# Kernel tuning notes

Measured on AMD Instinct MI355X. Metric: run time of the kernel, lower is better.

The kernel has to match this reference:

```python
import jax, jax.numpy as jnp
import numpy as np

B, T, C, H = 512, 512, 64, 128  # batch, timesteps, n_channel, n_hidden


def setup_inputs() -> dict:
    key = jax.random.key(0)
    k_x, k_wa, k_wi, k_we = jax.random.split(key, 4)
    x = jax.random.normal(k_x, (B, T, C), dtype=jnp.float32)
    # keras 'uniform' initializer: U(-0.05, 0.05)
    weight_att = jax.random.uniform(k_wa, (H, C, C), jnp.float32, -0.05, 0.05)
    weight_input = jax.random.uniform(k_wi, (H, C, C), jnp.float32, -0.05, 0.05)
    weight_e = jax.random.uniform(k_we, (H, C, C), jnp.float32, -0.05, 0.05)
    return {"x": x, "weight_att": weight_att, "weight_input": weight_input,
            "weight_e": weight_e}


def reference(x, weight_att, weight_input, weight_e):
    b, t, c = x.shape
    h = weight_input.shape[0]
    # initial attention state: ones / n_channel  -> [B, H, C]
    att0 = jnp.full((b, h, c), 1.0 / c, dtype=x.dtype)

    def step(att, x_t):
        # batch_mult(weight_input, x_t): out[b,h,c] = sum_k x_t[b,k] * W[h,c,k]
        a = jnp.einsum('bk,hck->bhc', x_t, weight_input)
        # batch_att_mult(weight_att, att): out[b,h,c] = sum_k att[b,h,k] * W[h,c,k]
        a = a + jnp.einsum('bhk,hck->bhc', att, weight_att)
        a = jnp.tanh(a)
        a = jnp.einsum('bhk,hck->bhc', a, weight_e)
        a = jax.nn.softmax(a, axis=-1)
        # reduce_sum(matmul(att [B,H,C], x [B,C,1]), -1) -> [B,H]
        out_t = jnp.einsum('bhc,bc->bh', a, x_t)
        return a, out_t

    xs = jnp.swapaxes(x, 0, 1)  # [T, B, C] for scan over time
    _, outs = jax.lax.scan(step, att0, xs)  # outs: [T, B, H]
    return jnp.swapaxes(outs, 0, 1)  # [B, T, H]
```

## Files before the change

kernel.cpp:

```cpp
#include <hip/hip_runtime.h>


constexpr int Bsz = 512, Tsz = 512, Csz = 64, Hsz = 128;

typedef __attribute__((ext_vector_type(8))) short short8;
typedef __attribute__((may_alias)) short8 short8m;
typedef __attribute__((ext_vector_type(4))) float f32x4;
typedef __attribute__((ext_vector_type(2))) unsigned int u32x2;
typedef __attribute__((may_alias)) u32x2 u32x2m;

#define LOG2E     1.44269504088896f
#define SCALE_CAT 2.88539008177793f

#define XT 0
#define AT 2304
#define YT 4608
#define OBF 6912
#define ROWB 144
#define OPITCH 20

__device__ __forceinline__ unsigned short f2bf_rn(float f) {
    return (unsigned short)((__float_as_uint(f) + 0x8000u) >> 16);
}
__device__ __forceinline__ unsigned int pkbf(float lo, float hi) {
    unsigned int r;
    asm("v_cvt_pk_bf16_f32 %0, %1, %2" : "=v"(r) : "v"(lo), "v"(hi));
    return r;
}
template<int CTRL>
__device__ __forceinline__ float dpp_add(float v) {
    int t = __builtin_amdgcn_update_dpp(0, __float_as_int(v), CTRL, 0xF, 0xF, true);
    return v + __int_as_float(t);
}
__device__ __forceinline__ float row_sum16(float v) {
    v = dpp_add<0x128>(v);
    v = dpp_add<0x124>(v);
    v = dpp_add<0x4E>(v);
    v = dpp_add<0xB1>(v);
    return v;
}

__global__ __launch_bounds__(256, 4)
void x_to_bf16_perm(const float* __restrict__ x, unsigned short* __restrict__ xb) {
    int g = blockIdx.x * 256 + threadIdx.x;
    int row = g >> 3, k = g & 7;
    int b = row >> 9, t = row & 511;
    const float* src = x + (size_t)row * 64;
    short8 f;
#pragma unroll
    for (int a = 0; a < 4; ++a) {
        float2 w = *(const float2*)(src + a * 16 + 2 * k);
        f[a]     = (short)f2bf_rn(w.x);
        f[4 + a] = (short)f2bf_rn(w.y);
    }
    size_t ob = ((size_t)((b >> 4) * Tsz + t) * 16 + (b & 15)) * 64 + k * 8;
    *(short8m*)(xb + ob) = f;
}

template<bool XPRE, bool OUTWS>
__global__ __launch_bounds__(256, 4)
void attn_scan(const float* __restrict__ xg,
               const unsigned short* __restrict__ xbg,
               const float* __restrict__ w_att,
               const float* __restrict__ w_in,
               const float* __restrict__ w_e,
               float* __restrict__ outg,
               float* __restrict__ outws)
{
    __shared__ __align__(16) unsigned short wefs[4096];
    __shared__ __align__(16) char priv[4][8192];

    const int h     = blockIdx.x & (Hsz - 1);
    const int btg   = blockIdx.x >> 7;
    const int wave  = threadIdx.x >> 6;
    const int lane  = threadIdx.x & 63;
    const int btile = btg * 4 + wave;
    const int b0    = btile * 16;

    const int l15  = lane & 15;
    const int quad = lane >> 4;
    const int rowb = quad * 4;
    const int sr   = lane >> 2;
    const int lq   = lane & 3;

    {
        const float* weh = w_e + (size_t)h * Csz * Csz;
#pragma unroll
        for (int i = 0; i < 2; ++i) {
            int tp = threadIdx.x * 2 + i;
            int ntks = tp >> 6, q = (tp >> 4) & 3, l = tp & 15;
            int ks = ntks & 1;
            int nt = ntks >> 1;
            int m = ks * 4 + q;
            const float* srcw = weh + (nt * 16 + l) * 64;
            short8 f;
#pragma unroll
            for (int j = 0; j < 8; ++j) {
                int kk = ((j & 3) << 4) + 2 * m + (j >> 2);
                f[j] = (short)f2bf_rn(srcw[kk] * LOG2E);
            }
            *(short8m*)(wefs + tp * 8) = f;
        }
    }

    short8 wcat[4][4];
    {
        const float* winh = w_in  + (size_t)h * Csz * Csz;
        const float* wath = w_att + (size_t)h * Csz * Csz;
#pragma unroll
        for (int nt = 0; nt < 4; ++nt) {
            const int c = nt * 16 + l15;
#pragma unroll
            for (int ks = 0; ks < 4; ++ks) {
                const float* srcw = ((ks < 2) ? winh : wath) + c * 64;
                const int m = (ks & 1) * 4 + quad;
                short8 f;
#pragma unroll
                for (int j = 0; j < 8; ++j) {
                    int kk = ((j & 3) << 4) + 2 * m + (j >> 2);
                    f[j] = (short)f2bf_rn(srcw[kk] * SCALE_CAT);
                }
                wcat[nt][ks] = f;
            }
        }
    }

    __syncthreads();

    char* wb  = priv[wave];
    char* wbr = wb + l15 * ROWB + quad * 16;
    char* wbd = wb + quad * (4 * ROWB) + l15 * 8;
    const unsigned short* wfp = wefs + quad * 128 + l15 * 8;
    float* ob = (float*)(wb + OBF);

    {
        short8 kinit;
#pragma unroll
        for (int j = 0; j < 8; ++j) kinit[j] = (short)0x3C80;
#pragma unroll
        for (int i = 0; i < 3; ++i) {
            int idx = i * 64 + lane;
            if (idx < 144) *(short8m*)(wb + AT + idx * 16) = kinit;
        }
    }

    {
        char* st = wb + XT + sr * ROWB + lq * 32;
        if (XPRE) {
            const unsigned short* xp = xbg + ((size_t)(btile * Tsz + 0) * 16 + sr) * 64 + lq * 16;
            *(short8m*)st        = *(const short8m*)xp;
            *(short8m*)(st + 16) = *(const short8m*)(xp + 8);
        } else {
            const float* xp = xg + ((size_t)(b0 + sr) * Tsz + 0) * 64 + lq * 4;
            float4 f0 = *(const float4*)(xp);
            float4 f1 = *(const float4*)(xp + 16);
            float4 f2 = *(const float4*)(xp + 32);
            float4 f3 = *(const float4*)(xp + 48);
            short8 lo, hi;
            lo[0]=(short)f2bf_rn(f0.x); lo[1]=(short)f2bf_rn(f1.x);
            lo[2]=(short)f2bf_rn(f2.x); lo[3]=(short)f2bf_rn(f3.x);
            lo[4]=(short)f2bf_rn(f0.y); lo[5]=(short)f2bf_rn(f1.y);
            lo[6]=(short)f2bf_rn(f2.y); lo[7]=(short)f2bf_rn(f3.y);
            hi[0]=(short)f2bf_rn(f0.z); hi[1]=(short)f2bf_rn(f1.z);
            hi[2]=(short)f2bf_rn(f2.z); hi[3]=(short)f2bf_rn(f3.z);
            hi[4]=(short)f2bf_rn(f0.w); hi[5]=(short)f2bf_rn(f1.w);
            hi[6]=(short)f2bf_rn(f2.w); hi[7]=(short)f2bf_rn(f3.w);
            *(short8m*)st = lo; *(short8m*)(st + 16) = hi;
        }
    }

    float rinv[4] = {1.f, 1.f, 1.f, 1.f};

    for (int t = 0; t < Tsz; ++t) {
        const int tn = (t < Tsz - 1) ? t + 1 : t;
        short8 pxa, pxb;
        float4 pf0, pf1, pf2, pf3;
        if (XPRE) {
            const unsigned short* xp = xbg + ((size_t)(btile * Tsz + tn) * 16 + sr) * 64 + lq * 16;
            pxa = *(const short8m*)xp;
            pxb = *(const short8m*)(xp + 8);
        } else {
            const float* xp = xg + ((size_t)(b0 + sr) * Tsz + tn) * 64 + lq * 4;
            pf0 = *(const float4*)(xp);      pf1 = *(const float4*)(xp + 16);
            pf2 = *(const float4*)(xp + 32); pf3 = *(const float4*)(xp + 48);
        }

        f32x4 vacc[4];
        {
            short8 aa0 = *(const short8m*)(wbr + AT);
            short8 aa1 = *(const short8m*)(wbr + AT + 64);
            f32x4 z = {0.f, 0.f, 0.f, 0.f};
#pragma unroll
            for (int nt = 0; nt < 4; ++nt) {
                vacc[nt] = __builtin_amdgcn_mfma_f32_16x16x32_bf16(aa0, wcat[nt][2], z, 0, 0, 0);
                vacc[nt] = __builtin_amdgcn_mfma_f32_16x16x32_bf16(aa1, wcat[nt][3], vacc[nt], 0, 0, 0);
            }
            short8 ax0 = *(const short8m*)(wbr + XT);
            short8 ax1 = *(const short8m*)(wbr + XT + 64);
#pragma unroll
            for (int nt = 0; nt < 4; ++nt)
#pragma unroll
                for (int rg = 0; rg < 4; ++rg)
                    vacc[nt][rg] *= rinv[rg];
#pragma unroll
            for (int nt = 0; nt < 4; ++nt) {
                vacc[nt] = __builtin_amdgcn_mfma_f32_16x16x32_bf16(ax0, wcat[nt][0], vacc[nt], 0, 0, 0);
                vacc[nt] = __builtin_amdgcn_mfma_f32_16x16x32_bf16(ax1, wcat[nt][1], vacc[nt], 0, 0, 0);
            }
        }

#pragma unroll
        for (int rg = 0; rg < 4; ++rg) {
            float E0 = __builtin_amdgcn_exp2f(vacc[0][rg]);
            float E1 = __builtin_amdgcn_exp2f(vacc[1][rg]);
            float E2 = __builtin_amdgcn_exp2f(vacc[2][rg]);
            float E3 = __builtin_amdgcn_exp2f(vacc[3][rg]);
            float y0 = fmaf(-2.f, __builtin_amdgcn_rcpf(E0 + 1.f), 1.f);
            float y1 = fmaf(-2.f, __builtin_amdgcn_rcpf(E1 + 1.f), 1.f);
            float y2 = fmaf(-2.f, __builtin_amdgcn_rcpf(E2 + 1.f), 1.f);
            float y3 = fmaf(-2.f, __builtin_amdgcn_rcpf(E3 + 1.f), 1.f);
            u32x2 d;
            d[0] = pkbf(y0, y1);
            d[1] = pkbf(y2, y3);
            *(u32x2m*)(wbd + YT + rg * ROWB) = d;
        }

        {
            short8 y0 = *(const short8m*)(wbr + YT);
            short8 y1 = *(const short8m*)(wbr + YT + 64);
            f32x4 z = {0.f, 0.f, 0.f, 0.f};
#pragma unroll
            for (int nt = 0; nt < 4; ++nt) {
                short8 w0 = *(const short8m*)(wfp + (nt * 2) * 512);
                short8 w1 = *(const short8m*)(wfp + (nt * 2 + 1) * 512);
                vacc[nt] = __builtin_amdgcn_mfma_f32_16x16x32_bf16(y0, w0, z, 0, 0, 0);
                vacc[nt] = __builtin_amdgcn_mfma_f32_16x16x32_bf16(y1, w1, vacc[nt], 0, 0, 0);
            }
        }

        float ssum[4], dsum[4];
#pragma unroll
        for (int rg = 0; rg < 4; ++rg) {
            u32x2 xd = *(const u32x2m*)(wbd + XT + rg * ROWB);
            float xv0 = __uint_as_float(xd[0] << 16);
            float xv1 = __uint_as_float(xd[0] & 0xffff0000u);
            float xv2 = __uint_as_float(xd[1] << 16);
            float xv3 = __uint_as_float(xd[1] & 0xffff0000u);
            float p0 = __builtin_amdgcn_exp2f(vacc[0][rg]);
            float p1 = __builtin_amdgcn_exp2f(vacc[1][rg]);
            float p2 = __builtin_amdgcn_exp2f(vacc[2][rg]);
            float p3 = __builtin_amdgcn_exp2f(vacc[3][rg]);
            u32x2 d;
            d[0] = pkbf(p0, p1);
            d[1] = pkbf(p2, p3);
            *(u32x2m*)(wbd + AT + rg * ROWB) = d;
            ssum[rg] = (p0 + p1) + (p2 + p3);
            dsum[rg] = fmaf(p0, xv0, fmaf(p1, xv1, fmaf(p2, xv2, p3 * xv3)));
        }
        float oval[4];
#pragma unroll
        for (int rg = 0; rg < 4; ++rg) {
            float s = row_sum16(ssum[rg]);
            float d = row_sum16(dsum[rg]);
            rinv[rg] = __builtin_amdgcn_rcpf(s);
            oval[rg] = d * rinv[rg];
        }

        if (l15 < 4) {
            float v = oval[0];
            v = (l15 == 1) ? oval[1] : v;
            v = (l15 == 2) ? oval[2] : v;
            v = (l15 == 3) ? oval[3] : v;
            if (OUTWS) {
                ob[(rowb + l15) * OPITCH + (t & 15)] = v;
            } else {
                outg[(size_t)(b0 + rowb + l15) * (Tsz * Hsz) + (size_t)t * Hsz + h] = v;
            }
        }
        if (OUTWS && ((t & 15) == 15)) {
            float4 v = *(const float4*)&ob[sr * OPITCH + lq * 4];
            *(float4*)&outws[((size_t)h * Bsz + b0 + sr) * Tsz + (t - 15) + lq * 4] = v;
        }

        char* st = wb + XT + sr * ROWB + lq * 32;
        if (XPRE) {
            *(short8m*)st = pxa; *(short8m*)(st + 16) = pxb;
        } else {
            short8 lo, hi;
            lo[0]=(short)f2bf_rn(pf0.x); lo[1]=(short)f2bf_rn(pf1.x);
            lo[2]=(short)f2bf_rn(pf2.x); lo[3]=(short)f2bf_rn(pf3.x);
            lo[4]=(short)f2bf_rn(pf0.y); lo[5]=(short)f2bf_rn(pf1.y);
            lo[6]=(short)f2bf_rn(pf2.y); lo[7]=(short)f2bf_rn(pf3.y);
            hi[0]=(short)f2bf_rn(pf0.z); hi[1]=(short)f2bf_rn(pf1.z);
            hi[2]=(short)f2bf_rn(pf2.z); hi[3]=(short)f2bf_rn(pf3.z);
            hi[4]=(short)f2bf_rn(pf0.w); hi[5]=(short)f2bf_rn(pf1.w);
            hi[6]=(short)f2bf_rn(pf2.w); hi[7]=(short)f2bf_rn(pf3.w);
            *(short8m*)st = lo; *(short8m*)(st + 16) = hi;
        }
    }
}

__global__ __launch_bounds__(256, 4)
void out_transpose(const float* __restrict__ ws, float* __restrict__ outg) {
    __shared__ float tile[64][65];
    const int t0 = blockIdx.x * 64;
    const int h0 = blockIdx.y * 64;
    const int b  = blockIdx.z;
    const int tx = threadIdx.x & 63;
    const int wy = threadIdx.x >> 6;
#pragma unroll
    for (int i = 0; i < 16; ++i) {
        int hr = wy * 16 + i;
        tile[hr][tx] = ws[((size_t)(h0 + hr) * Bsz + b) * Tsz + t0 + tx];
    }
    __syncthreads();
#pragma unroll
    for (int i = 0; i < 16; ++i) {
        int tt = wy * 16 + i;
        outg[((size_t)b * Tsz + t0 + tt) * Hsz + h0 + tx] = tile[tx][tt];
    }
}

extern "C" void kernel_launch(void* const* d_in, const int* in_sizes, int n_in,
                              void* d_out, int out_size, void* d_ws, size_t ws_size,
                              hipStream_t stream) {
    const float* x     = (const float*)d_in[0];
    const float* w_att = (const float*)d_in[1];
    const float* w_in  = (const float*)d_in[2];
    const float* w_e   = (const float*)d_in[3];
    float* out = (float*)d_out;

    const size_t XB = (size_t)Bsz * Tsz * Csz * sizeof(unsigned short);
    const size_t OB = (size_t)Bsz * Tsz * Hsz * sizeof(float);
    unsigned short* xb  = (unsigned short*)d_ws;
    float*          ows = (float*)((char*)d_ws + XB);

    const int xblocks = Bsz * Tsz * 8 / 256;
    dim3 scan_grid(Hsz * (Bsz / 64));

    if (ws_size >= XB + OB) {
        x_to_bf16_perm<<<xblocks, 256, 0, stream>>>(x, xb);
        attn_scan<true, true><<<scan_grid, 256, 0, stream>>>(x, xb, w_att, w_in, w_e, out, ows);
        dim3 tg(Tsz / 64, Hsz / 64, Bsz);
        out_transpose<<<tg, 256, 0, stream>>>(ows, out);
    } else if (ws_size >= XB) {
        x_to_bf16_perm<<<xblocks, 256, 0, stream>>>(x, xb);
        attn_scan<true, false><<<scan_grid, 256, 0, stream>>>(x, xb, w_att, w_in, w_e, out, nullptr);
    } else {
        attn_scan<false, false><<<scan_grid, 256, 0, stream>>>(x, nullptr, w_att, w_in, w_e, out, nullptr);
    }
}
```

Before: 1.501 ms.

## Compute softmax sums and x-dot via MFMA, keep x fragments in registers

Replaces the DPP row reductions for the softmax denominator and the x-weighted sum with extra MFMA calls. These multiply the bf16 probability tile by a ones vector and by the x fragment, and only the diagonal lanes are used for the output. The x tile is now loaded straight into MFMA operand registers each step instead of being staged through LDS, which shrinks the per-wave LDS area and drops the LDS output staging buffer. Outputs are written directly per step rather than batched into float4 stores. The sums now come from bf16-rounded probabilities, and most of the dot-product MFMA output is discarded.

```diff
diff --git a/kernel.cpp b/kernel.cpp
--- a/kernel.cpp
+++ b/kernel.cpp
@@ -12,12 +12,9 @@
 #define LOG2E     1.44269504088896f
 #define SCALE_CAT 2.88539008177793f
 
-#define XT 0
-#define AT 2304
-#define YT 4608
-#define OBF 6912
+#define AT 0
+#define YT 2304
 #define ROWB 144
-#define OPITCH 20
 
 __device__ __forceinline__ unsigned short f2bf_rn(float f) {
     return (unsigned short)((__float_as_uint(f) + 0x8000u) >> 16);
@@ -26,18 +23,6 @@
     unsigned int r;
     asm("v_cvt_pk_bf16_f32 %0, %1, %2" : "=v"(r) : "v"(lo), "v"(hi));
     return r;
-}
-template<int CTRL>
-__device__ __forceinline__ float dpp_add(float v) {
-    int t = __builtin_amdgcn_update_dpp(0, __float_as_int(v), CTRL, 0xF, 0xF, true);
-    return v + __int_as_float(t);
-}
-__device__ __forceinline__ float row_sum16(float v) {
-    v = dpp_add<0x128>(v);
-    v = dpp_add<0x124>(v);
-    v = dpp_add<0x4E>(v);
-    v = dpp_add<0xB1>(v);
-    return v;
 }
 
 __global__ __launch_bounds__(256, 4)
@@ -55,6 +40,22 @@
     }
     size_t ob = ((size_t)((b >> 4) * Tsz + t) * 16 + (b & 15)) * 64 + k * 8;
     *(short8m*)(xb + ob) = f;
+}
+
+__device__ __forceinline__ void load_xfrag_f32(const float* src, int quad,
+                                               short8& f0, short8& f1) {
+#pragma unroll
+    for (int hh = 0; hh < 2; ++hh) {
+        short8 f;
+        const int K = hh * 8 + quad * 2;
+#pragma unroll
+        for (int m = 0; m < 4; ++m) {
+            float2 w = *(const float2*)(src + K + 16 * m);
+            f[m]     = (short)f2bf_rn(w.x);
+            f[m + 4] = (short)f2bf_rn(w.y);
+        }
+        if (hh == 0) f0 = f; else f1 = f;
+    }
 }
 
 template<bool XPRE, bool OUTWS>
@@ -68,7 +69,7 @@
                float* __restrict__ outws)
 {
     __shared__ __align__(16) unsigned short wefs[4096];
-    __shared__ __align__(16) char priv[4][8192];
+    __shared__ __align__(16) char priv[4][4608];
 
     const int h     = blockIdx.x & (Hsz - 1);
     const int btg   = blockIdx.x >> 7;
@@ -80,8 +81,6 @@
     const int l15  = lane & 15;
     const int quad = lane >> 4;
     const int rowb = quad * 4;
-    const int sr   = lane >> 2;
-    const int lq   = lane & 3;
 
     {
         const float* weh = w_e + (size_t)h * Csz * Csz;
@@ -131,7 +130,10 @@
     char* wbr = wb + l15 * ROWB + quad * 16;
     char* wbd = wb + quad * (4 * ROWB) + l15 * 8;
     const unsigned short* wfp = wefs + quad * 128 + l15 * 8;
-    float* ob = (float*)(wb + OBF);
+
+    short8 ones8;
+#pragma unroll
+    for (int j = 0; j < 8; ++j) ones8[j] = (short)0x3F80;
 
     {
         short8 kinit;
@@ -144,45 +146,35 @@
         }
     }
 
-    {
-        char* st = wb + XT + sr * ROWB + lq * 32;
-        if (XPRE) {
-            const unsigned short* xp = xbg + ((size_t)(btile * Tsz + 0) * 16 + sr) * 64 + lq * 16;
-            *(short8m*)st        = *(const short8m*)xp;
-            *(short8m*)(st + 16) = *(const short8m*)(xp + 8);
-        } else {
-            const float* xp = xg + ((size_t)(b0 + sr) * Tsz + 0) * 64 + lq * 4;
-            float4 f0 = *(const float4*)(xp);
-            float4 f1 = *(const float4*)(xp + 16);
-            float4 f2 = *(const float4*)(xp + 32);
-            float4 f3 = *(const float4*)(xp + 48);
-            short8 lo, hi;
-            lo[0]=(short)f2bf_rn(f0.x); lo[1]=(short)f2bf_rn(f1.x);
-            lo[2]=(short)f2bf_rn(f2.x); lo[3]=(short)f2bf_rn(f3.x);
-            lo[4]=(short)f2bf_rn(f0.y); lo[5]=(short)f2bf_rn(f1.y);
-            lo[6]=(short)f2bf_rn(f2.y); lo[7]=(short)f2bf_rn(f3.y);
-            hi[0]=(short)f2bf_rn(f0.z); hi[1]=(short)f2bf_rn(f1.z);
-            hi[2]=(short)f2bf_rn(f2.z); hi[3]=(short)f2bf_rn(f3.z);
-            hi[4]=(short)f2bf_rn(f0.w); hi[5]=(short)f2bf_rn(f1.w);
-            hi[6]=(short)f2bf_rn(f2.w); hi[7]=(short)f2bf_rn(f3.w);
-            *(short8m*)st = lo; *(short8m*)(st + 16) = hi;
-        }
+    const unsigned short* xfp = nullptr;
+    if (XPRE)
+        xfp = xbg + (size_t)btile * Tsz * 1024 + l15 * 64 + quad * 8;
+
+    const int  k3     = l15 & 3;
+    const int  orow   = rowb + k3;
+    const bool isdiag = ((l15 >> 2) == quad);
+    float* op;
+    if (OUTWS) op = outws + ((size_t)h * Bsz + b0 + orow) * Tsz;
+    else       op = outg + (size_t)(b0 + orow) * (Tsz * Hsz) + h;
+
+    short8 axc0, axc1;
+    if (XPRE) {
+        axc0 = *(const short8m*)(xfp);
+        axc1 = *(const short8m*)(xfp + 32);
+    } else {
+        load_xfrag_f32(xg + ((size_t)(b0 + l15) * Tsz) * 64, quad, axc0, axc1);
     }
 
     float rinv[4] = {1.f, 1.f, 1.f, 1.f};
 
     for (int t = 0; t < Tsz; ++t) {
         const int tn = (t < Tsz - 1) ? t + 1 : t;
-        short8 pxa, pxb;
-        float4 pf0, pf1, pf2, pf3;
+        short8 axn0, axn1;
         if (XPRE) {
-            const unsigned short* xp = xbg + ((size_t)(btile * Tsz + tn) * 16 + sr) * 64 + lq * 16;
-            pxa = *(const short8m*)xp;
-            pxb = *(const short8m*)(xp + 8);
+            axn0 = *(const short8m*)(xfp + (size_t)tn * 1024);
+            axn1 = *(const short8m*)(xfp + (size_t)tn * 1024 + 32);
         } else {
-            const float* xp = xg + ((size_t)(b0 + sr) * Tsz + tn) * 64 + lq * 4;
-            pf0 = *(const float4*)(xp);      pf1 = *(const float4*)(xp + 16);
-            pf2 = *(const float4*)(xp + 32); pf3 = *(const float4*)(xp + 48);
+            load_xfrag_f32(xg + ((size_t)(b0 + l15) * Tsz + tn) * 64, quad, axn0, axn1);
         }
 
         f32x4 vacc[4];
@@ -195,8 +187,6 @@
                 vacc[nt] = __builtin_amdgcn_mfma_f32_16x16x32_bf16(aa0, wcat[nt][2], z, 0, 0, 0);
                 vacc[nt] = __builtin_amdgcn_mfma_f32_16x16x32_bf16(aa1, wcat[nt][3], vacc[nt], 0, 0, 0);
             }
-            short8 ax0 = *(const short8m*)(wbr + XT);
-            short8 ax1 = *(const short8m*)(wbr + XT + 64);
 #pragma unroll
             for (int nt = 0; nt < 4; ++nt)
 #pragma unroll
@@ -204,8 +194,8 @@
                     vacc[nt][rg] *= rinv[rg];
 #pragma unroll
             for (int nt = 0; nt < 4; ++nt) {
-                vacc[nt] = __builtin_amdgcn_mfma_f32_16x16x32_bf16(ax0, wcat[nt][0], vacc[nt], 0, 0, 0);
-                vacc[nt] = __builtin_amdgcn_mfma_f32_16x16x32_bf16(ax1, wcat[nt][1], vacc[nt], 0, 0, 0);
+                vacc[nt] = __builtin_amdgcn_mfma_f32_16x16x32_bf16(axc0, wcat[nt][0], vacc[nt], 0, 0, 0);
+                vacc[nt] = __builtin_amdgcn_mfma_f32_16x16x32_bf16(axc1, wcat[nt][1], vacc[nt], 0, 0, 0);
             }
         }
 
@@ -238,14 +228,8 @@
             }
         }
 
-        float ssum[4], dsum[4];
 #pragma unroll
         for (int rg = 0; rg < 4; ++rg) {
-            u32x2 xd = *(const u32x2m*)(wbd + XT + rg * ROWB);
-            float xv0 = __uint_as_float(xd[0] << 16);
-            float xv1 = __uint_as_float(xd[0] & 0xffff0000u);
-            float xv2 = __uint_as_float(xd[1] << 16);
-            float xv3 = __uint_as_float(xd[1] & 0xffff0000u);
             float p0 = __builtin_amdgcn_exp2f(vacc[0][rg]);
             float p1 = __builtin_amdgcn_exp2f(vacc[1][rg]);
             float p2 = __builtin_amdgcn_exp2f(vacc[2][rg]);
@@ -254,49 +238,37 @@
             d[0] = pkbf(p0, p1);
             d[1] = pkbf(p2, p3);
             *(u32x2m*)(wbd + AT + rg * ROWB) = d;
-            ssum[rg] = (p0 + p1) + (p2 + p3);
-            dsum[rg] = fmaf(p0, xv0, fmaf(p1, xv1, fmaf(p2, xv2, p3 * xv3)));
-        }
-        float oval[4];
-#pragma unroll
-        for (int rg = 0; rg < 4; ++rg) {
-            float s = row_sum16(ssum[rg]);
-            float d = row_sum16(dsum[rg]);
-            rinv[rg] = __builtin_amdgcn_rcpf(s);
-            oval[rg] = d * rinv[rg];
-        }
-
-        if (l15 < 4) {
-            float v = oval[0];
-            v = (l15 == 1) ? oval[1] : v;
-            v = (l15 == 2) ? oval[2] : v;
-            v = (l15 == 3) ? oval[3] : v;
-            if (OUTWS) {
-                ob[(rowb + l15) * OPITCH + (t & 15)] = v;
-            } else {
-                outg[(size_t)(b0 + rowb + l15) * (Tsz * Hsz) + (size_t)t * Hsz + h] = v;
-            }
-        }
-        if (OUTWS && ((t & 15) == 15)) {
-            float4 v = *(const float4*)&ob[sr * OPITCH + lq * 4];
-            *(float4*)&outws[((size_t)h * Bsz + b0 + sr) * Tsz + (t - 15) + lq * 4] = v;
-        }
-
-        char* st = wb + XT + sr * ROWB + lq * 32;
-        if (XPRE) {
-            *(short8m*)st = pxa; *(short8m*)(st + 16) = pxb;
-        } else {
-            short8 lo, hi;
-            lo[0]=(short)f2bf_rn(pf0.x); lo[1]=(short)f2bf_rn(pf1.x);
-            lo[2]=(short)f2bf_rn(pf2.x); lo[3]=(short)f2bf_rn(pf3.x);
-            lo[4]=(short)f2bf_rn(pf0.y); lo[5]=(short)f2bf_rn(pf1.y);
-            lo[6]=(short)f2bf_rn(pf2.y); lo[7]=(short)f2bf_rn(pf3.y);
-            hi[0]=(short)f2bf_rn(pf0.z); hi[1]=(short)f2bf_rn(pf1.z);
-            hi[2]=(short)f2bf_rn(pf2.z); hi[3]=(short)f2bf_rn(pf3.z);
-            hi[4]=(short)f2bf_rn(pf0.w); hi[5]=(short)f2bf_rn(pf1.w);
-            hi[6]=(short)f2bf_rn(pf2.w); hi[7]=(short)f2bf_rn(pf3.w);
-            *(short8m*)st = lo; *(short8m*)(st + 16) = hi;
-        }
+        }
+
+        {
+            short8 pa0 = *(const short8m*)(wbr + AT);
+            short8 pa1 = *(const short8m*)(wbr + AT + 64);
+            f32x4 z = {0.f, 0.f, 0.f, 0.f};
+            f32x4 sacc = __builtin_amdgcn_mfma_f32_16x16x32_bf16(pa0, ones8, z, 0, 0, 0);
+            sacc = __builtin_amdgcn_mfma_f32_16x16x32_bf16(pa1, ones8, sacc, 0, 0, 0);
+            f32x4 dacc = __builtin_amdgcn_mfma_f32_16x16x32_bf16(pa0, axc0, z, 0, 0, 0);
+            dacc = __builtin_amdgcn_mfma_f32_16x16x32_bf16(pa1, axc1, dacc, 0, 0, 0);
+
+            rinv[0] = __builtin_amdgcn_rcpf(sacc[0]);
+            rinv[1] = __builtin_amdgcn_rcpf(sacc[1]);
+            rinv[2] = __builtin_amdgcn_rcpf(sacc[2]);
+            rinv[3] = __builtin_amdgcn_rcpf(sacc[3]);
+
+            float dv = dacc[0];
+            dv = (k3 == 1) ? dacc[1] : dv;
+            dv = (k3 == 2) ? dacc[2] : dv;
+            dv = (k3 == 3) ? dacc[3] : dv;
+            float rv = rinv[0];
+            rv = (k3 == 1) ? rinv[1] : rv;
+            rv = (k3 == 2) ? rinv[2] : rv;
+            rv = (k3 == 3) ? rinv[3] : rv;
+            if (isdiag) {
+                if (OUTWS) op[t] = dv * rv;
+                else       op[(size_t)t * Hsz] = dv * rv;
+            }
+        }
+
+        axc0 = axn0; axc1 = axn1;
     }
 }
 
```

After: 1.352 ms. 1.11x faster.
